# Kernel optimization log

Measured on AMD Instinct MI355X. Metric: run time of the kernel, lower is better.

Reference implementation:

```python
import jax, jax.numpy as jnp
import numpy as np

DIM = 96
HEADS = 6
WS = 8                      # window_size
OWS = int(WS * 0.5) + WS    # overlap_win_size = 12
PAD = (OWS - WS) // 2       # 2
Dd = Hh = Ww = 24
B = 1
L = Dd * Hh * Ww
MLP_H = DIM * 2
TBL = (WS + OWS - 1) ** 3   # 6859 relative-position-bias entries


def setup_inputs() -> dict:
    key = jax.random.key(0)
    ks = jax.random.split(key, 8)
    def n(k, shape, s=0.02):
        return jax.random.normal(k, shape, jnp.float32) * s
    return {
        "x": jax.random.normal(ks[0], (B, L, DIM), jnp.float32),
        "ln1_w": jnp.ones((DIM,), jnp.float32),
        "ln1_b": jnp.zeros((DIM,), jnp.float32),
        "qkv_w": n(ks[1], (3 * DIM, DIM)),
        "qkv_b": jnp.zeros((3 * DIM,), jnp.float32),
        "rpb": n(ks[2], (TBL, HEADS)),
        "proj_w": n(ks[3], (DIM, DIM)),
        "proj_b": jnp.zeros((DIM,), jnp.float32),
        "ln2_w": jnp.ones((DIM,), jnp.float32),
        "ln2_b": jnp.zeros((DIM,), jnp.float32),
        "fc1_w": n(ks[4], (MLP_H, DIM)),
        "fc1_b": jnp.zeros((MLP_H,), jnp.float32),
        "fc2_w": n(ks[5], (DIM, MLP_H)),
        "fc2_b": jnp.zeros((DIM,), jnp.float32),
        "rpi": jax.random.randint(ks[6], (WS ** 3, OWS ** 3), 0, TBL),
        "D": Dd, "H": Hh, "W": Ww,
    }


def _ln(x, w, b):
    m = jnp.mean(x, -1, keepdims=True)
    v = jnp.var(x, -1, keepdims=True)
    return (x - m) / jnp.sqrt(v + 1e-5) * w + b


def _ocab3d(x, ln1_w, ln1_b, qkv_w, qkv_b, rpb, proj_w, proj_b,
            ln2_w, ln2_b, fc1_w, fc1_b, fc2_w, fc2_b, rpi, D, H, W):
    Bz, Lz, C = x.shape
    hd = C // HEADS
    scale = hd ** -0.5
    shortcut = x

    xn = _ln(x, ln1_w, ln1_b).reshape(Bz, D, H, W, C)
    qkv = xn @ qkv_w.T + qkv_b                   # [B,D,H,W,3C]
    q = qkv[..., :C]
    kv = qkv[..., C:]                            # cat(k, v) on channels, [B,D,H,W,2C]

    nD, nH, nW = D // WS, H // WS, W // WS
    nw = nD * nH * nW

    # non-overlapping query windows -> [B*nw, WS^3, C]
    qw = q.reshape(Bz, nD, WS, nH, WS, nW, WS, C)
    qw = qw.transpose(0, 1, 3, 5, 2, 4, 6, 7).reshape(Bz * nw, WS ** 3, C)

    # overlapping kv windows via pad + strided gather (mirrors F.pad + unfold)
    kvp = jnp.pad(kv, ((0, 0), (PAD, PAD), (PAD, PAD), (PAD, PAD), (0, 0)))
    idx_d = (jnp.arange(nD) * WS)[:, None] + jnp.arange(OWS)[None, :]
    idx_h = (jnp.arange(nH) * WS)[:, None] + jnp.arange(OWS)[None, :]
    idx_w = (jnp.arange(nW) * WS)[:, None] + jnp.arange(OWS)[None, :]
    kw = kvp[:, idx_d]                 # [B,nD,OWS,Hp,Wp,2C]
    kw = kw[:, :, :, idx_h]            # [B,nD,OWS,nH,OWS,Wp,2C]
    kw = kw[:, :, :, :, :, idx_w]      # [B,nD,OWS,nH,OWS,nW,OWS,2C]
    kw = kw.transpose(0, 1, 3, 5, 2, 4, 6, 7).reshape(Bz * nw, OWS ** 3, 2 * C)
    kk, vv = kw[..., :C], kw[..., C:]

    qh = qw.reshape(-1, WS ** 3, HEADS, hd).transpose(0, 2, 1, 3) * scale
    kh = kk.reshape(-1, OWS ** 3, HEADS, hd).transpose(0, 2, 1, 3)
    vh = vv.reshape(-1, OWS ** 3, HEADS, hd).transpose(0, 2, 1, 3)

    attn = jnp.einsum('bhqd,bhkd->bhqk', qh, kh)               # [B*nw,H,512,1728]
    bias = rpb[rpi.reshape(-1)].reshape(WS ** 3, OWS ** 3, HEADS).transpose(2, 0, 1)
    attn = jax.nn.softmax(attn + bias[None], axis=-1)
    out = jnp.einsum('bhqk,bhkd->bhqd', attn, vh)
    out = out.transpose(0, 2, 1, 3).reshape(Bz * nw, WS ** 3, C)

    # window reverse -> [B, L, C]
    out = out.reshape(Bz, nD, nH, nW, WS, WS, WS, C)
    out = out.transpose(0, 1, 4, 2, 5, 3, 6, 7).reshape(Bz, D * H * W, C)

    x2 = out @ proj_w.T + proj_b + shortcut
    h1 = jax.nn.gelu(_ln(x2, ln2_w, ln2_b) @ fc1_w.T + fc1_b, approximate=False)
    return x2 + (h1 @ fc2_w.T + fc2_b)


def reference(x, ln1_w, ln1_b, qkv_w, qkv_b, rpb, proj_w, proj_b,
              ln2_w, ln2_b, fc1_w, fc1_b, fc2_w, fc2_b, rpi, D, H, W):
    return _ocab3d(x, ln1_w, ln1_b, qkv_w, qkv_b, rpb, proj_w, proj_b,
                   ln2_w, ln2_b, fc1_w, fc1_b, fc2_w, fc2_b, rpi, D, H, W)
```

## Files before the change

kernel.cpp:

```cpp
#include <hip/hip_runtime.h>
#include <math.h>

#define DIMC   96
#define NHEADS 6
#define HD     16
#define WSZ    8
#define OWSZ   12
#define PADW   2
#define DD     24
#define LTOK   13824
#define NWIN   27
#define NKEY   1728
#define NROW   512
#define MLPH   192
#define PDIM   28
#define PD3    21952
#define TBL    6859
#define LSTR   82944
#define AOSTR  1327104
#define LOG2E  1.4426950408889634f

typedef __attribute__((ext_vector_type(4))) short bf16x4;
typedef __attribute__((ext_vector_type(8))) short bf16x8;
typedef __attribute__((ext_vector_type(4))) float f32x4;

__device__ __forceinline__ unsigned short bfround(float f) {
    unsigned u = __float_as_uint(f);
    return (unsigned short)((u + 0x7FFFu + ((u >> 16) & 1u)) >> 16);
}
__device__ __forceinline__ unsigned bfpack(float a, float b) {
    unsigned ua = __float_as_uint(a), ub = __float_as_uint(b);
    ua = (ua + 0x7FFFu + ((ua >> 16) & 1u)) >> 16;
    ub = (ub + 0x7FFFu + ((ub >> 16) & 1u)) >> 16;
    return ua | (ub << 16);
}
__device__ __forceinline__ uint4 pack8(const float* v) {
    uint4 u;
    u.x = bfpack(v[0], v[1]); u.y = bfpack(v[2], v[3]);
    u.z = bfpack(v[4], v[5]); u.w = bfpack(v[6], v[7]);
    return u;
}
__device__ __forceinline__ bf16x4 pack4(f32x4 p) {
    union { uint2 u; bf16x4 v; } r;
    r.u.x = __builtin_amdgcn_perm(__float_as_uint(p[1]), __float_as_uint(p[0]), 0x07060302u);
    r.u.y = __builtin_amdgcn_perm(__float_as_uint(p[3]), __float_as_uint(p[2]), 0x07060302u);
    return r.v;
}
__device__ __forceinline__ f32x4 cvt4(uint2 b) {
    f32x4 c;
    c[0] = __uint_as_float(b.x << 16);
    c[1] = __uint_as_float(b.x & 0xffff0000u);
    c[2] = __uint_as_float(b.y << 16);
    c[3] = __uint_as_float(b.y & 0xffff0000u);
    return c;
}
__device__ __forceinline__ f32x4 mfma16(bf16x4 a, bf16x4 b, f32x4 c) {
#if __has_builtin(__builtin_amdgcn_mfma_f32_16x16x16bf16_1k)
    return __builtin_amdgcn_mfma_f32_16x16x16bf16_1k(a, b, c, 0, 0, 0);
#else
    bf16x8 a8 = {a[0], a[1], a[2], a[3], 0, 0, 0, 0};
    bf16x8 b8 = {b[0], b[1], b[2], b[3], 0, 0, 0, 0};
    return __builtin_amdgcn_mfma_f32_16x16x32_bf16(a8, b8, c, 0, 0, 0);
#endif
}
__device__ __forceinline__ f32x4 mfma32k(bf16x8 a, bf16x8 b, f32x4 c) {
    return __builtin_amdgcn_mfma_f32_16x16x32_bf16(a, b, c, 0, 0, 0);
}
__device__ __forceinline__ float fexp2(float x) {
#if __has_builtin(__builtin_amdgcn_exp2f)
    return __builtin_amdgcn_exp2f(x);
#else
    return exp2f(x);
#endif
}

#define QKVB 1296
#define ZB   515
#define WPB  45
#define BIASB 216
__global__ __launch_bounds__(256) void qkvz_kernel(
        const float* __restrict__ X, const float* __restrict__ W,
        const float* __restrict__ bias, const float* __restrict__ lnw,
        const float* __restrict__ lnb,
        const float* __restrict__ projw, const float* __restrict__ fc1w,
        const float* __restrict__ fc2w,
        const int* __restrict__ rpi, const float* __restrict__ rpb,
        unsigned short* __restrict__ q16, unsigned short* __restrict__ kvp2,
        uint4* __restrict__ wpack, unsigned short* __restrict__ biasP) {
    __shared__ uint4 Af4[2 * 3 * 4 * 16];
    __shared__ uint4 Bf4[6 * 3 * 4 * 16];
    int bx = blockIdx.x, tid = threadIdx.x;

    if (bx >= QKVB + ZB + WPB) {
        int b2 = bx - (QKVB + ZB + WPB);
        int c  = b2 % 27;
        int qp = b2 / 27;
        int quart = qp >> 1, qt = qp & 1;
        int wavep = tid >> 6, quadp = (tid >> 4) & 3, m16p = tid & 15;
        int q = quart * 128 + wavep * 32 + qt * 16 + m16p;
        const int* rp = rpi + (long)q * NKEY + c * 64 + quadp * 8;
        #pragma unroll
        for (int kt = 0; kt < 4; ++kt) {
            int4 t = *(const int4*)(rp + (kt >> 1) * 32 + (kt & 1) * 4);
            const float2* p0 = (const float2*)(rpb + (long)t.x * 6);
            const float2* p1 = (const float2*)(rpb + (long)t.y * 6);
            const float2* p2 = (const float2*)(rpb + (long)t.z * 6);
            const float2* p3 = (const float2*)(rpb + (long)t.w * 6);
            #pragma unroll
            for (int hp = 0; hp < 3; ++hp) {
                float2 a0 = p0[hp], a1 = p1[hp], a2 = p2[hp], a3 = p3[hp];
                uint2 ua, ub;
                ua.x = bfpack(a0.x * LOG2E, a1.x * LOG2E);
                ua.y = bfpack(a2.x * LOG2E, a3.x * LOG2E);
                ub.x = bfpack(a0.y * LOG2E, a1.y * LOG2E);
                ub.y = bfpack(a2.y * LOG2E, a3.y * LOG2E);
                *(uint2*)(biasP + ((long)((2*hp)   * 4 + quart) * 27 + c) * 8192
                          + qt * 4096 + tid * 16 + kt * 4) = ua;
                *(uint2*)(biasP + ((long)((2*hp+1) * 4 + quart) * 27 + c) * 8192
                          + qt * 4096 + tid * 16 + kt * 4) = ub;
            }
        }
        return;
    }
    if (bx >= QKVB + ZB) {
        int u = (bx - QKVB - ZB) * 256 + tid;
        if (u < 5760) {
            int p = (u < 1152) ? u : (u < 3456 ? (u - 1152) % 1152 : (u - 3456) % 1152);
            int nn = p & 15, r = p >> 4, qg = r & 3, r2 = r >> 2;
            int kt = r2 % 3, ct = r2 / 3;
            int n = ct * 16 + nn, g = kt * 4 + qg;
            const float* src;
            if (u < 1152)      src = projw + n * 96 + g * 8;
            else if (u < 3456) { int nc = (u - 1152) / 1152; src = fc1w + (long)(nc * 96 + n) * 96 + g * 8; }
            else               { int kh = (u - 3456) / 1152; src = fc2w + (long)n * 192 + kh * 96 + g * 8; }
            const float4* s4 = (const float4*)src;
            float v[8];
            float4 t0 = s4[0], t1 = s4[1];
            v[0]=t0.x; v[1]=t0.y; v[2]=t0.z; v[3]=t0.w;
            v[4]=t1.x; v[5]=t1.y; v[6]=t1.z; v[7]=t1.w;
            wpack[u] = pack8(v);
        }
        return;
    }
    if (bx >= QKVB) {
        int t = (bx - QKVB) * 256 + tid;
        if (t < 21952 * 6) {
            int head = t / PD3, pos = t % PD3;
            int d = pos / 784, h = (pos / 28) % 28, w = pos % 28;
            if (d < 2 || d >= 26 || h < 2 || h >= 26 || w < 2 || w >= 26) {
                uint4* p = (uint4*)(kvp2 + ((long)head * PD3 + pos) * 32);
                uint4 z = make_uint4(0, 0, 0, 0);
                p[0] = z; p[1] = z; p[2] = z; p[3] = z;
            }
        }
        return;
    }

    int nc   = bx % 3;
    int row0 = (bx / 3) * 32;

    if (tid < 128) {
        int row = tid >> 2, part = tid & 3;
        int rt = row >> 4, mm = row & 15;
        float v[24];
        const float4* xp = (const float4*)(X + (long)(row0 + row) * 96 + part * 24);
        float s = 0.f, sq = 0.f;
        #pragma unroll
        for (int i = 0; i < 6; ++i) {
            float4 t = xp[i];
            v[i*4+0] = t.x; v[i*4+1] = t.y; v[i*4+2] = t.z; v[i*4+3] = t.w;
            s  += t.x + t.y + t.z + t.w;
            sq += t.x*t.x + t.y*t.y + t.z*t.z + t.w*t.w;
        }
        s  += __shfl_xor(s, 1);  s  += __shfl_xor(s, 2);
        sq += __shfl_xor(sq, 1); sq += __shfl_xor(sq, 2);
        float mean = s * (1.f / 96.f);
        float inv  = rsqrtf(sq * (1.f / 96.f) - mean * mean + 1e-5f);
        const float4* wp = (const float4*)(lnw + part * 24);
        const float4* bp = (const float4*)(lnb + part * 24);
        #pragma unroll
        for (int i = 0; i < 6; ++i) {
            float4 wv = wp[i], bv = bp[i];
            v[i*4+0] = (v[i*4+0] - mean) * inv * wv.x + bv.x;
            v[i*4+1] = (v[i*4+1] - mean) * inv * wv.y + bv.y;
            v[i*4+2] = (v[i*4+2] - mean) * inv * wv.z + bv.z;
            v[i*4+3] = (v[i*4+3] - mean) * inv * wv.w + bv.w;
        }
        #pragma unroll
        for (int gg = 0; gg < 3; ++gg) {
            int g = part * 3 + gg;
            int kt = g >> 2, qq = g & 3;
            Af4[((rt * 3 + kt) * 4 + qq) * 16 + mm] = pack8(v + gg * 8);
        }
    }
    for (int idx = tid; idx < 96 * 12; idx += 256) {
        int n = idx / 12;
        int g = idx % 12;
        const float4* wp = (const float4*)(W + (long)(nc * 96 + n) * 96 + g * 8);
        float v[8];
        float4 t0 = wp[0], t1 = wp[1];
        v[0]=t0.x; v[1]=t0.y; v[2]=t0.z; v[3]=t0.w;
        v[4]=t1.x; v[5]=t1.y; v[6]=t1.z; v[7]=t1.w;
        int ct = n >> 4, nn = n & 15, kt = g >> 2, qg = g & 3;
        Bf4[((ct * 3 + kt) * 4 + qg) * 16 + nn] = pack8(v);
    }
    __syncthreads();

    int wave = tid >> 6, lane = tid & 63;
    int qq = lane >> 4, mI = lane & 15;
    int rt = wave & 1, cg = wave >> 1;

    f32x4 acc[3];
    #pragma unroll
    for (int j = 0; j < 3; ++j) acc[j] = (f32x4){0.f, 0.f, 0.f, 0.f};
    #pragma unroll
    for (int kt = 0; kt < 3; ++kt) {
        bf16x8 a = *(const bf16x8*)&Af4[((rt * 3 + kt) * 4 + qq) * 16 + mI];
        #pragma unroll
        for (int j = 0; j < 3; ++j) {
            bf16x8 b = *(const bf16x8*)&Bf4[(((cg * 3 + j) * 3 + kt) * 4 + qq) * 16 + mI];
            acc[j] = __builtin_amdgcn_mfma_f32_16x16x32_bf16(a, b, acc[j], 0, 0, 0);
        }
    }

    float bv[3];
    #pragma unroll
    for (int j = 0; j < 3; ++j) bv[j] = bias[nc * 96 + (cg * 3 + j) * 16 + mI];
    #pragma unroll
    for (int r = 0; r < 4; ++r) {
        int row = row0 + rt * 16 + qq * 4 + r;
        if (nc == 0) {
            unsigned short* op = q16 + (long)row * 96;
            #pragma unroll
            for (int j = 0; j < 3; ++j)
                op[(cg * 3 + j) * 16 + mI] = bfround(0.25f * LOG2E * (acc[j][r] + bv[j]));
        } else {
            int d = row / 576, hh = (row / 24) % 24, w2 = row % 24;
            long pos = ((long)(d + 2) * 28 + (hh + 2)) * 28 + (w2 + 2);
            #pragma unroll
            for (int j = 0; j < 3; ++j) {
                int head = cg * 3 + j;
                kvp2[((long)head * PD3 + pos) * 32 +
                     (nc == 2 ? 16 : 0) + mI] = bfround(acc[j][r] + bv[j]);
            }
        }
    }
}

#define KSTR 20
#define VKP  66

#define ATTN_STEP(P, BCUR, BNXT)                                              \
    {                                                                         \
        bool more = (cc + (P) + 1 < cn);                                      \
        if (more) stgn = *kvaddr(c0 + cc + (P) + 1);                          \
        __syncthreads();                                                      \
        bf16x4 kf[4];                                                         \
        _Pragma("unroll")                                                     \
        for (int kt = 0; kt < 4; ++kt)                                        \
            kf[kt] = *(const bf16x4*)&Ks[(P)][(kt * 16 + m16) * KSTR + quad * 4]; \
        bf16x8 vb0 = *(const bf16x8*)&Vt[(P)][m16 * VKP + quad * 8];          \
        bf16x8 vb1 = *(const bf16x8*)&Vt[(P)][m16 * VKP + 32 + quad * 8];     \
        f32x4 S[2][4];                                                        \
        _Pragma("unroll")                                                     \
        for (int qt = 0; qt < 2; ++qt) {                                      \
            _Pragma("unroll")                                                 \
            for (int kt = 0; kt < 4; ++kt) {                                  \
                uint4 bj = BCUR[qt][kt >> 1];                                 \
                uint2 bb = (kt & 1) ? make_uint2(bj.z, bj.w)                  \
                                    : make_uint2(bj.x, bj.y);                 \
                S[qt][kt] = mfma16(kf[kt], qf[qt], cvt4(bb));                 \
            }                                                                 \
        }                                                                     \
        if (more) {                                                           \
            const unsigned short* bp = bbase + (long)(c0 + cc + (P) + 1) * 8192 \
                                       + tid * 16;                            \
            _Pragma("unroll")                                                 \
            for (int qt = 0; qt < 2; ++qt) {                                  \
                BNXT[qt][0] = *(const uint4*)(bp + qt * 4096);                \
                BNXT[qt][1] = *(const uint4*)(bp + qt * 4096 + 8);            \
            }                                                                 \
        }                                                                     \
        bf16x8 P8[2][2];                                                      \
        _Pragma("unroll")                                                     \
        for (int qt = 0; qt < 2; ++qt) {                                      \
            _Pragma("unroll")                                                 \
            for (int u = 0; u < 2; ++u) {                                     \
                f32x4 p0, p1;                                                 \
                _Pragma("unroll")                                             \
                for (int r = 0; r < 4; ++r) {                                 \
                    p0[r] = fexp2(S[qt][2 * u][r]);                           \
                    p1[r] = fexp2(S[qt][2 * u + 1][r]);                       \
                }                                                             \
                union { struct { bf16x4 lo, hi; } h; bf16x8 v; } uu;          \
                uu.h.lo = pack4(p0); uu.h.hi = pack4(p1);                     \
                P8[qt][u] = uu.v;                                             \
                lacc[qt] = mfma32k(P8[qt][u], ones8, lacc[qt]);               \
            }                                                                 \
        }                                                                     \
        o[0] = mfma32k(P8[0][0], vb0, o[0]);                                  \
        o[1] = mfma32k(P8[1][0], vb0, o[1]);                                  \
        o[0] = mfma32k(P8[0][1], vb1, o[0]);                                  \
        o[1] = mfma32k(P8[1][1], vb1, o[1]);                                  \
        if (more) writeLDS((P) ^ 1, stgn);                                    \
    }

__global__ __launch_bounds__(256, 3) void attn_kernel(
        const unsigned short* __restrict__ q, const unsigned short* __restrict__ kvp2,
        const unsigned short* __restrict__ biasP, float* __restrict__ ao,
        float* __restrict__ lbuf) {
    __shared__ unsigned short Ks[2][64 * KSTR];
    __shared__ unsigned short Vt[2][16 * VKP];
    int bid = blockIdx.x;
    int w = bid / 48, rem = bid % 48;
    int head = rem >> 3;
    int quart = (rem >> 1) & 3, half = rem & 1;
    int wd8 = (w / 9) * 8, wh8 = ((w / 3) % 3) * 8, ww8 = (w % 3) * 8;
    int tid = threadIdx.x, wave = tid >> 6, lane = tid & 63;
    int quad = lane >> 4, m16 = lane & 15;
    int key = tid >> 2, part = tid & 3;
    int c0 = half ? 13 : 0;
    int cn = half ? 14 : 13;

    int skey = (key & 35) | ((key & 4) << 2) | ((key >> 1) & 12);

    auto kvaddr = [&](int c) -> const uint4* {
        int jg = c * 64 + key;
        int i = jg / 144, jh = (jg / 12) % 12, jw = jg % 12;
        long sp = ((long)(wd8 + i) * PDIM + (wh8 + jh)) * PDIM + (ww8 + jw);
        return (const uint4*)(kvp2 + ((long)head * PD3 + sp) * 32 + part * 8);
    };
    auto writeLDS = [&](int b, uint4 v) {
        if (part < 2) {
            *(uint2*)(&Ks[b][skey * KSTR + part * 8])     = make_uint2(v.x, v.y);
            *(uint2*)(&Ks[b][skey * KSTR + part * 8 + 4]) = make_uint2(v.z, v.w);
        } else {
            int d0 = (part - 2) * 8;
            unsigned short* vp = &Vt[b][d0 * VKP + key];
            vp[0 * VKP] = (unsigned short)(v.x);
            vp[1 * VKP] = (unsigned short)(v.x >> 16);
            vp[2 * VKP] = (unsigned short)(v.y);
            vp[3 * VKP] = (unsigned short)(v.y >> 16);
            vp[4 * VKP] = (unsigned short)(v.z);
            vp[5 * VKP] = (unsigned short)(v.z >> 16);
            vp[6 * VKP] = (unsigned short)(v.w);
            vp[7 * VKP] = (unsigned short)(v.w >> 16);
        }
    };

    bf16x4 qf[2];
    #pragma unroll
    for (int qt = 0; qt < 2; ++qt) {
        int ql = quart * 128 + wave * 32 + qt * 16 + m16;
        int ld = ql >> 6, lh = (ql >> 3) & 7, lw = ql & 7;
        int g = ((wd8 + ld) * 24 + (wh8 + lh)) * 24 + (ww8 + lw);
        qf[qt] = *(const bf16x4*)(q + (long)g * 96 + head * 16 + quad * 4);
    }

    const unsigned short* bbase = biasP + ((long)(head * 4 + quart) * 27) * 8192;
    uint4 bb0[2][2], bb1[2][2];
    {
        const unsigned short* bp = bbase + (long)c0 * 8192 + tid * 16;
        #pragma unroll
        for (int qt = 0; qt < 2; ++qt) {
            bb0[qt][0] = *(const uint4*)(bp + qt * 4096);
            bb0[qt][1] = *(const uint4*)(bp + qt * 4096 + 8);
        }
    }

    writeLDS(0, *kvaddr(c0));

    const bf16x8 ones8 = {(short)0x3F80, (short)0x3F80, (short)0x3F80, (short)0x3F80,
                          (short)0x3F80, (short)0x3F80, (short)0x3F80, (short)0x3F80};
    f32x4 o[2], lacc[2];
    o[0] = (f32x4){0.f,0.f,0.f,0.f}; o[1] = (f32x4){0.f,0.f,0.f,0.f};
    lacc[0] = o[0]; lacc[1] = o[1];
    uint4 stgn;

    for (int cc = 0; cc < cn; cc += 2) {
        ATTN_STEP(0, bb0, bb1)
        if (cc + 1 < cn) ATTN_STEP(1, bb1, bb0)
    }

    float* aout = ao + (long)half * AOSTR;
    float* lout = lbuf + (long)half * LSTR;
    #pragma unroll
    for (int qt = 0; qt < 2; ++qt) {
        #pragma unroll
        for (int r = 0; r < 4; ++r) {
            int ql = quart * 128 + wave * 32 + qt * 16 + quad * 4 + r;
            int ld = ql >> 6, lh = (ql >> 3) & 7, lw = ql & 7;
            int g = ((wd8 + ld) * 24 + (wh8 + lh)) * 24 + (ww8 + lw);
            aout[(long)g * 96 + head * 16 + m16] = o[qt][r];
            if (m16 == 0) lout[g * 6 + head] = lacc[qt][r];
        }
    }
}

#define X2S 100
__global__ __launch_bounds__(512) void mlp_kernel(
        const float* __restrict__ ao0, const float* __restrict__ ao1,
        const float* __restrict__ lbuf, const uint4* __restrict__ wpack,
        const float* __restrict__ projb, const float* __restrict__ x,
        const float* __restrict__ ln2w, const float* __restrict__ ln2b,
        const float* __restrict__ fc1b, const float* __restrict__ fc2b,
        float* __restrict__ out) {
    __shared__ uint4 Ws[5760];
    __shared__ uint4 Af4[4 * 3 * 4 * 16];
    __shared__ float x2s[64 * X2S];
    __shared__ unsigned short h16[64 * 192];
    int tid = threadIdx.x;
    int row0 = blockIdx.x * 64;
    int wave = tid >> 6, lane = tid & 63;
    int qq = lane >> 4, mI = lane & 15;
    int rt = wave & 3, cg = wave >> 2;

    for (int idx = tid; idx < 5760; idx += 512) Ws[idx] = wpack[idx];

    if (tid < 256) {
        int row = tid >> 2, part = tid & 3;
        int rtA = row >> 4, mm = row & 15;
        int grow = row0 + row;
        const float4* a0 = (const float4*)(ao0 + (long)grow * 96 + part * 24);
        const float4* a1 = (const float4*)(ao1 + (long)grow * 96 + part * 24);
        int ha = (part * 3) >> 1, hb = ha + 1;
        float inva = 1.f / (lbuf[grow*6 + ha] + lbuf[LSTR + grow*6 + ha]);
        float invb = 1.f / (lbuf[grow*6 + hb] + lbuf[LSTR + grow*6 + hb]);
        float v[24];
        #pragma unroll
        for (int i = 0; i < 6; ++i) {
            float4 u0 = a0[i], u1 = a1[i];
            #pragma unroll
            for (int j = 0; j < 4; ++j) {
                int gc = part * 24 + i * 4 + j;
                float lv = ((gc >> 4) == ha) ? inva : invb;
                float s = (j==0?u0.x+u1.x : j==1?u0.y+u1.y : j==2?u0.z+u1.z : u0.w+u1.w);
                v[i*4+j] = s * lv;
            }
        }
        #pragma unroll
        for (int gg = 0; gg < 3; ++gg) {
            int g = part * 3 + gg;
            int kt = g >> 2, q4 = g & 3;
            Af4[((rtA * 3 + kt) * 4 + q4) * 16 + mm] = pack8(v + gg * 8);
        }
    }
    __syncthreads();

    {
        f32x4 acc[3];
        #pragma unroll
        for (int j = 0; j < 3; ++j) acc[j] = (f32x4){0.f,0.f,0.f,0.f};
        #pragma unroll
        for (int kt = 0; kt < 3; ++kt) {
            bf16x8 a = *(const bf16x8*)&Af4[((rt * 3 + kt) * 4 + qq) * 16 + mI];
            #pragma unroll
            for (int j = 0; j < 3; ++j) {
                bf16x8 b = *(const bf16x8*)&Ws[(((cg * 3 + j) * 3 + kt) * 4 + qq) * 16 + mI];
                acc[j] = __builtin_amdgcn_mfma_f32_16x16x32_bf16(a, b, acc[j], 0, 0, 0);
            }
        }
        float bv[3];
        #pragma unroll
        for (int j = 0; j < 3; ++j) bv[j] = projb[(cg * 3 + j) * 16 + mI];
        #pragma unroll
        for (int r = 0; r < 4; ++r) {
            int row = rt * 16 + qq * 4 + r;
            int grow = row0 + row;
            #pragma unroll
            for (int j = 0; j < 3; ++j) {
                int col = (cg * 3 + j) * 16 + mI;
                x2s[row * X2S + col] = acc[j][r] + bv[j] + x[(long)grow * 96 + col];
            }
        }
    }
    __syncthreads();

    if (tid < 256) {
        int row = tid >> 2, part = tid & 3;
        int rtA = row >> 4, mm = row & 15;
        float v[24];
        const float4* xp = (const float4*)(x2s + row * X2S + part * 24);
        float s = 0.f, sq = 0.f;
        #pragma unroll
        for (int i = 0; i < 6; ++i) {
            float4 t = xp[i];
            v[i*4+0] = t.x; v[i*4+1] = t.y; v[i*4+2] = t.z; v[i*4+3] = t.w;
            s  += t.x + t.y + t.z + t.w;
            sq += t.x*t.x + t.y*t.y + t.z*t.z + t.w*t.w;
        }
        s  += __shfl_xor(s, 1);  s  += __shfl_xor(s, 2);
        sq += __shfl_xor(sq, 1); sq += __shfl_xor(sq, 2);
        float mean = s * (1.f / 96.f);
        float inv  = rsqrtf(sq * (1.f / 96.f) - mean * mean + 1e-5f);
        const float4* wp = (const float4*)(ln2w + part * 24);
        const float4* bp = (const float4*)(ln2b + part * 24);
        #pragma unroll
        for (int i = 0; i < 6; ++i) {
            float4 wv = wp[i], bv = bp[i];
            v[i*4+0] = (v[i*4+0] - mean) * inv * wv.x + bv.x;
            v[i*4+1] = (v[i*4+1] - mean) * inv * wv.y + bv.y;
            v[i*4+2] = (v[i*4+2] - mean) * inv * wv.z + bv.z;
            v[i*4+3] = (v[i*4+3] - mean) * inv * wv.w + bv.w;
        }
        #pragma unroll
        for (int gg = 0; gg < 3; ++gg) {
            int g = part * 3 + gg;
            int kt = g >> 2, q4 = g & 3;
            Af4[((rtA * 3 + kt) * 4 + q4) * 16 + mm] = pack8(v + gg * 8);
        }
    }
    __syncthreads();

    #pragma unroll
    for (int nc = 0; nc < 2; ++nc) {
        f32x4 acc[3];
        #pragma unroll
        for (int j = 0; j < 3; ++j) acc[j] = (f32x4){0.f,0.f,0.f,0.f};
        #pragma unroll
        for (int kt = 0; kt < 3; ++kt) {
            bf16x8 a = *(const bf16x8*)&Af4[((rt * 3 + kt) * 4 + qq) * 16 + mI];
            #pragma unroll
            for (int j = 0; j < 3; ++j) {
                bf16x8 b = *(const bf16x8*)&Ws[1152 + nc * 1152 +
                               (((cg * 3 + j) * 3 + kt) * 4 + qq) * 16 + mI];
                acc[j] = __builtin_amdgcn_mfma_f32_16x16x32_bf16(a, b, acc[j], 0, 0, 0);
            }
        }
        float bv[3];
        #pragma unroll
        for (int j = 0; j < 3; ++j) bv[j] = fc1b[nc * 96 + (cg * 3 + j) * 16 + mI];
        #pragma unroll
        for (int r = 0; r < 4; ++r) {
            int row = rt * 16 + qq * 4 + r;
            #pragma unroll
            for (int j = 0; j < 3; ++j) {
                int col = nc * 96 + (cg * 3 + j) * 16 + mI;
                float v = acc[j][r] + bv[j];
                float g = 0.5f * v * (1.f + erff(v * 0.70710678f));
                int fi = (((row >> 4) * 6 + (col >> 5)) * 4 + ((col >> 3) & 3)) * 16 + (row & 15);
                h16[fi * 8 + (col & 7)] = bfround(g);
            }
        }
    }
    __syncthreads();

    f32x4 acc2[3];
    #pragma unroll
    for (int j = 0; j < 3; ++j) acc2[j] = (f32x4){0.f,0.f,0.f,0.f};
    #pragma unroll
    for (int kh = 0; kh < 2; ++kh) {
        #pragma unroll
        for (int kt = 0; kt < 3; ++kt) {
            int ktA = kh * 3 + kt;
            bf16x8 a = *(const bf16x8*)&h16[(((rt * 6 + ktA) * 4 + qq) * 16 + mI) * 8];
            #pragma unroll
            for (int j = 0; j < 3; ++j) {
                bf16x8 b = *(const bf16x8*)&Ws[3456 + kh * 1152 +
                               (((cg * 3 + j) * 3 + kt) * 4 + qq) * 16 + mI];
                acc2[j] = __builtin_amdgcn_mfma_f32_16x16x32_bf16(a, b, acc2[j], 0, 0, 0);
            }
        }
    }
    float bv[3];
    #pragma unroll
    for (int j = 0; j < 3; ++j) bv[j] = fc2b[(cg * 3 + j) * 16 + mI];
    #pragma unroll
    for (int r = 0; r < 4; ++r) {
        int row = rt * 16 + qq * 4 + r;
        int grow = row0 + row;
        #pragma unroll
        for (int j = 0; j < 3; ++j) {
            int col = (cg * 3 + j) * 16 + mI;
            out[(long)grow * 96 + col] = acc2[j][r] + bv[j] + x2s[row * X2S + col];
        }
    }
}

extern "C" void kernel_launch(void* const* d_in, const int* in_sizes, int n_in,
                              void* d_out, int out_size, void* d_ws, size_t ws_size,
                              hipStream_t stream) {
    const float* x     = (const float*)d_in[0];
    const float* ln1w  = (const float*)d_in[1];
    const float* ln1b  = (const float*)d_in[2];
    const float* qkvw  = (const float*)d_in[3];
    const float* qkvb  = (const float*)d_in[4];
    const float* rpb   = (const float*)d_in[5];
    const float* projw = (const float*)d_in[6];
    const float* projb = (const float*)d_in[7];
    const float* ln2w  = (const float*)d_in[8];
    const float* ln2b  = (const float*)d_in[9];
    const float* fc1w  = (const float*)d_in[10];
    const float* fc1b  = (const float*)d_in[11];
    const float* fc2w  = (const float*)d_in[12];
    const float* fc2b  = (const float*)d_in[13];
    const int*   rpi   = (const int*)d_in[14];
    float* outp = (float*)d_out;

    float* ws = (float*)d_ws;
    float*          aop    = ws;
    unsigned short* q16    = (unsigned short*)(ws + 2654208);
    unsigned short* kvp16  = (unsigned short*)(ws + 3317760);
    unsigned short* biasPh = (unsigned short*)(ws + 5425152);
    float*          lbuf   = ws + 10733568;
    uint4*          wpack  = (uint4*)(ws + 10899456);

    qkvz_kernel<<<QKVB + ZB + WPB + BIASB, 256, 0, stream>>>(
        x, qkvw, qkvb, ln1w, ln1b, projw, fc1w, fc2w, rpi, rpb,
        q16, kvp16, wpack, biasPh);
    attn_kernel<<<NWIN * NHEADS * 4 * 2, 256, 0, stream>>>(q16, kvp16, biasPh, aop, lbuf);
    mlp_kernel<<<LTOK / 64, 512, 0, stream>>>(aop, aop + AOSTR, lbuf, wpack, projb, x,
                                              ln2w, ln2b, fc1b, fc2b, outp);
}
```

Baseline: 158.8 us.

## Split attention blocks per query tile, read MLP weights from global, vectorize bias gather

```diff
diff --git a/kernel.cpp b/kernel.cpp
--- a/kernel.cpp
+++ b/kernel.cpp
@@ -102,23 +102,34 @@
         #pragma unroll
         for (int kt = 0; kt < 4; ++kt) {
             int4 t = *(const int4*)(rp + (kt >> 1) * 32 + (kt & 1) * 4);
-            const float2* p0 = (const float2*)(rpb + (long)t.x * 6);
-            const float2* p1 = (const float2*)(rpb + (long)t.y * 6);
-            const float2* p2 = (const float2*)(rpb + (long)t.z * 6);
-            const float2* p3 = (const float2*)(rpb + (long)t.w * 6);
-            #pragma unroll
-            for (int hp = 0; hp < 3; ++hp) {
-                float2 a0 = p0[hp], a1 = p1[hp], a2 = p2[hp], a3 = p3[hp];
-                uint2 ua, ub;
-                ua.x = bfpack(a0.x * LOG2E, a1.x * LOG2E);
-                ua.y = bfpack(a2.x * LOG2E, a3.x * LOG2E);
-                ub.x = bfpack(a0.y * LOG2E, a1.y * LOG2E);
-                ub.y = bfpack(a2.y * LOG2E, a3.y * LOG2E);
-                *(uint2*)(biasP + ((long)((2*hp)   * 4 + quart) * 27 + c) * 8192
-                          + qt * 4096 + tid * 16 + kt * 4) = ua;
-                *(uint2*)(biasP + ((long)((2*hp+1) * 4 + quart) * 27 + c) * 8192
-                          + qt * 4096 + tid * 16 + kt * 4) = ub;
-            }
+            const float* b0 = rpb + (long)t.x * 6;
+            const float* b1 = rpb + (long)t.y * 6;
+            const float* b2p = rpb + (long)t.z * 6;
+            const float* b3 = rpb + (long)t.w * 6;
+            float4 q0 = *(const float4*)b0; float2 r0 = *(const float2*)(b0 + 4);
+            float4 q1 = *(const float4*)b1; float2 r1 = *(const float2*)(b1 + 4);
+            float4 q2 = *(const float4*)b2p; float2 r2 = *(const float2*)(b2p + 4);
+            float4 q3 = *(const float4*)b3; float2 r3 = *(const float2*)(b3 + 4);
+            long ob = qt * 4096 + tid * 16 + kt * 4;
+            uint2 ua, ub;
+            ua.x = bfpack(q0.x * LOG2E, q1.x * LOG2E);
+            ua.y = bfpack(q2.x * LOG2E, q3.x * LOG2E);
+            ub.x = bfpack(q0.y * LOG2E, q1.y * LOG2E);
+            ub.y = bfpack(q2.y * LOG2E, q3.y * LOG2E);
+            *(uint2*)(biasP + ((long)(0 * 4 + quart) * 27 + c) * 8192 + ob) = ua;
+            *(uint2*)(biasP + ((long)(1 * 4 + quart) * 27 + c) * 8192 + ob) = ub;
+            ua.x = bfpack(q0.z * LOG2E, q1.z * LOG2E);
+            ua.y = bfpack(q2.z * LOG2E, q3.z * LOG2E);
+            ub.x = bfpack(q0.w * LOG2E, q1.w * LOG2E);
+            ub.y = bfpack(q2.w * LOG2E, q3.w * LOG2E);
+            *(uint2*)(biasP + ((long)(2 * 4 + quart) * 27 + c) * 8192 + ob) = ua;
+            *(uint2*)(biasP + ((long)(3 * 4 + quart) * 27 + c) * 8192 + ob) = ub;
+            ua.x = bfpack(r0.x * LOG2E, r1.x * LOG2E);
+            ua.y = bfpack(r2.x * LOG2E, r3.x * LOG2E);
+            ub.x = bfpack(r0.y * LOG2E, r1.y * LOG2E);
+            ub.y = bfpack(r2.y * LOG2E, r3.y * LOG2E);
+            *(uint2*)(biasP + ((long)(4 * 4 + quart) * 27 + c) * 8192 + ob) = ua;
+            *(uint2*)(biasP + ((long)(5 * 4 + quart) * 27 + c) * 8192 + ob) = ub;
         }
         return;
     }
@@ -261,60 +272,49 @@
             kf[kt] = *(const bf16x4*)&Ks[(P)][(kt * 16 + m16) * KSTR + quad * 4]; \
         bf16x8 vb0 = *(const bf16x8*)&Vt[(P)][m16 * VKP + quad * 8];          \
         bf16x8 vb1 = *(const bf16x8*)&Vt[(P)][m16 * VKP + 32 + quad * 8];     \
-        f32x4 S[2][4];                                                        \
+        f32x4 S[4];                                                           \
         _Pragma("unroll")                                                     \
-        for (int qt = 0; qt < 2; ++qt) {                                      \
-            _Pragma("unroll")                                                 \
-            for (int kt = 0; kt < 4; ++kt) {                                  \
-                uint4 bj = BCUR[qt][kt >> 1];                                 \
-                uint2 bb = (kt & 1) ? make_uint2(bj.z, bj.w)                  \
-                                    : make_uint2(bj.x, bj.y);                 \
-                S[qt][kt] = mfma16(kf[kt], qf[qt], cvt4(bb));                 \
-            }                                                                 \
+        for (int kt = 0; kt < 4; ++kt) {                                      \
+            uint4 bj = BCUR[kt >> 1];                                         \
+            uint2 bb = (kt & 1) ? make_uint2(bj.z, bj.w)                      \
+                                : make_uint2(bj.x, bj.y);                     \
+            S[kt] = mfma16(kf[kt], qf, cvt4(bb));                             \
         }                                                                     \
         if (more) {                                                           \
             const unsigned short* bp = bbase + (long)(c0 + cc + (P) + 1) * 8192 \
                                        + tid * 16;                            \
+            BNXT[0] = *(const uint4*)(bp);                                    \
+            BNXT[1] = *(const uint4*)(bp + 8);                                \
+        }                                                                     \
+        bf16x8 P8[2];                                                         \
+        _Pragma("unroll")                                                     \
+        for (int u = 0; u < 2; ++u) {                                         \
+            f32x4 p0, p1;                                                     \
             _Pragma("unroll")                                                 \
-            for (int qt = 0; qt < 2; ++qt) {                                  \
-                BNXT[qt][0] = *(const uint4*)(bp + qt * 4096);                \
-                BNXT[qt][1] = *(const uint4*)(bp + qt * 4096 + 8);            \
+            for (int r = 0; r < 4; ++r) {                                     \
+                p0[r] = fexp2(S[2 * u][r]);                                   \
+                p1[r] = fexp2(S[2 * u + 1][r]);                               \
             }                                                                 \
+            union { struct { bf16x4 lo, hi; } h; bf16x8 v; } uu;              \
+            uu.h.lo = pack4(p0); uu.h.hi = pack4(p1);                         \
+            P8[u] = uu.v;                                                     \
+            lacc = mfma32k(P8[u], ones8, lacc);                               \
         }                                                                     \
-        bf16x8 P8[2][2];                                                      \
-        _Pragma("unroll")                                                     \
-        for (int qt = 0; qt < 2; ++qt) {                                      \
-            _Pragma("unroll")                                                 \
-            for (int u = 0; u < 2; ++u) {                                     \
-                f32x4 p0, p1;                                                 \
-                _Pragma("unroll")                                             \
-                for (int r = 0; r < 4; ++r) {                                 \
-                    p0[r] = fexp2(S[qt][2 * u][r]);                           \
-                    p1[r] = fexp2(S[qt][2 * u + 1][r]);                       \
-                }                                                             \
-                union { struct { bf16x4 lo, hi; } h; bf16x8 v; } uu;          \
-                uu.h.lo = pack4(p0); uu.h.hi = pack4(p1);                     \
-                P8[qt][u] = uu.v;                                             \
-                lacc[qt] = mfma32k(P8[qt][u], ones8, lacc[qt]);               \
-            }                                                                 \
-        }                                                                     \
-        o[0] = mfma32k(P8[0][0], vb0, o[0]);                                  \
-        o[1] = mfma32k(P8[1][0], vb0, o[1]);                                  \
-        o[0] = mfma32k(P8[0][1], vb1, o[0]);                                  \
-        o[1] = mfma32k(P8[1][1], vb1, o[1]);                                  \
+        o = mfma32k(P8[0], vb0, o);                                           \
+        o = mfma32k(P8[1], vb1, o);                                           \
         if (more) writeLDS((P) ^ 1, stgn);                                    \
     }
 
-__global__ __launch_bounds__(256, 3) void attn_kernel(
+__global__ __launch_bounds__(256, 4) void attn_kernel(
         const unsigned short* __restrict__ q, const unsigned short* __restrict__ kvp2,
         const unsigned short* __restrict__ biasP, float* __restrict__ ao,
         float* __restrict__ lbuf) {
     __shared__ unsigned short Ks[2][64 * KSTR];
     __shared__ unsigned short Vt[2][16 * VKP];
     int bid = blockIdx.x;
-    int w = bid / 48, rem = bid % 48;
-    int head = rem >> 3;
-    int quart = (rem >> 1) & 3, half = rem & 1;
+    int w = bid / 96, rem = bid % 96;
+    int head = rem >> 4;
+    int quart = (rem >> 2) & 3, qt = (rem >> 1) & 1, half = rem & 1;
     int wd8 = (w / 9) * 8, wh8 = ((w / 3) % 3) * 8, ww8 = (w % 3) * 8;
     int tid = threadIdx.x, wave = tid >> 6, lane = tid & 63;
     int quad = lane >> 4, m16 = lane & 15;
@@ -348,33 +348,29 @@
         }
     };
 
-    bf16x4 qf[2];
-    #pragma unroll
-    for (int qt = 0; qt < 2; ++qt) {
+    bf16x4 qf;
+    {
         int ql = quart * 128 + wave * 32 + qt * 16 + m16;
         int ld = ql >> 6, lh = (ql >> 3) & 7, lw = ql & 7;
         int g = ((wd8 + ld) * 24 + (wh8 + lh)) * 24 + (ww8 + lw);
-        qf[qt] = *(const bf16x4*)(q + (long)g * 96 + head * 16 + quad * 4);
-    }
-
-    const unsigned short* bbase = biasP + ((long)(head * 4 + quart) * 27) * 8192;
-    uint4 bb0[2][2], bb1[2][2];
+        qf = *(const bf16x4*)(q + (long)g * 96 + head * 16 + quad * 4);
+    }
+
+    const unsigned short* bbase = biasP + ((long)(head * 4 + quart) * 27) * 8192
+                                  + qt * 4096;
+    uint4 bb0[2], bb1[2];
     {
         const unsigned short* bp = bbase + (long)c0 * 8192 + tid * 16;
-        #pragma unroll
-        for (int qt = 0; qt < 2; ++qt) {
-            bb0[qt][0] = *(const uint4*)(bp + qt * 4096);
-            bb0[qt][1] = *(const uint4*)(bp + qt * 4096 + 8);
-        }
+        bb0[0] = *(const uint4*)(bp);
+        bb0[1] = *(const uint4*)(bp + 8);
     }
 
     writeLDS(0, *kvaddr(c0));
 
     const bf16x8 ones8 = {(short)0x3F80, (short)0x3F80, (short)0x3F80, (short)0x3F80,
                           (short)0x3F80, (short)0x3F80, (short)0x3F80, (short)0x3F80};
-    f32x4 o[2], lacc[2];
-    o[0] = (f32x4){0.f,0.f,0.f,0.f}; o[1] = (f32x4){0.f,0.f,0.f,0.f};
-    lacc[0] = o[0]; lacc[1] = o[1];
+    f32x4 o = (f32x4){0.f,0.f,0.f,0.f};
+    f32x4 lacc = (f32x4){0.f,0.f,0.f,0.f};
     uint4 stgn;
 
     for (int cc = 0; cc < cn; cc += 2) {
@@ -385,15 +381,12 @@
     float* aout = ao + (long)half * AOSTR;
     float* lout = lbuf + (long)half * LSTR;
     #pragma unroll
-    for (int qt = 0; qt < 2; ++qt) {
-        #pragma unroll
-        for (int r = 0; r < 4; ++r) {
-            int ql = quart * 128 + wave * 32 + qt * 16 + quad * 4 + r;
-            int ld = ql >> 6, lh = (ql >> 3) & 7, lw = ql & 7;
-            int g = ((wd8 + ld) * 24 + (wh8 + lh)) * 24 + (ww8 + lw);
-            aout[(long)g * 96 + head * 16 + m16] = o[qt][r];
-            if (m16 == 0) lout[g * 6 + head] = lacc[qt][r];
-        }
+    for (int r = 0; r < 4; ++r) {
+        int ql = quart * 128 + wave * 32 + qt * 16 + quad * 4 + r;
+        int ld = ql >> 6, lh = (ql >> 3) & 7, lw = ql & 7;
+        int g = ((wd8 + ld) * 24 + (wh8 + lh)) * 24 + (ww8 + lw);
+        aout[(long)g * 96 + head * 16 + m16] = o[r];
+        if (m16 == 0) lout[g * 6 + head] = lacc[r];
     }
 }
 
@@ -405,7 +398,6 @@
         const float* __restrict__ ln2w, const float* __restrict__ ln2b,
         const float* __restrict__ fc1b, const float* __restrict__ fc2b,
         float* __restrict__ out) {
-    __shared__ uint4 Ws[5760];
     __shared__ uint4 Af4[4 * 3 * 4 * 16];
     __shared__ float x2s[64 * X2S];
     __shared__ unsigned short h16[64 * 192];
@@ -414,8 +406,6 @@
     int wave = tid >> 6, lane = tid & 63;
     int qq = lane >> 4, mI = lane & 15;
     int rt = wave & 3, cg = wave >> 2;
-
-    for (int idx = tid; idx < 5760; idx += 512) Ws[idx] = wpack[idx];
 
     if (tid < 256) {
         int row = tid >> 2, part = tid & 3;
@@ -456,7 +446,7 @@
             bf16x8 a = *(const bf16x8*)&Af4[((rt * 3 + kt) * 4 + qq) * 16 + mI];
             #pragma unroll
             for (int j = 0; j < 3; ++j) {
-                bf16x8 b = *(const bf16x8*)&Ws[(((cg * 3 + j) * 3 + kt) * 4 + qq) * 16 + mI];
+                bf16x8 b = *(const bf16x8*)&wpack[(((cg * 3 + j) * 3 + kt) * 4 + qq) * 16 + mI];
                 acc[j] = __builtin_amdgcn_mfma_f32_16x16x32_bf16(a, b, acc[j], 0, 0, 0);
             }
         }
@@ -522,7 +512,7 @@
             bf16x8 a = *(const bf16x8*)&Af4[((rt * 3 + kt) * 4 + qq) * 16 + mI];
             #pragma unroll
             for (int j = 0; j < 3; ++j) {
-                bf16x8 b = *(const bf16x8*)&Ws[1152 + nc * 1152 +
+                bf16x8 b = *(const bf16x8*)&wpack[1152 + nc * 1152 +
                                (((cg * 3 + j) * 3 + kt) * 4 + qq) * 16 + mI];
                 acc[j] = __builtin_amdgcn_mfma_f32_16x16x32_bf16(a, b, acc[j], 0, 0, 0);
             }
@@ -556,7 +546,7 @@
             bf16x8 a = *(const bf16x8*)&h16[(((rt * 6 + ktA) * 4 + qq) * 16 + mI) * 8];
             #pragma unroll
             for (int j = 0; j < 3; ++j) {
-                bf16x8 b = *(const bf16x8*)&Ws[3456 + kh * 1152 +
+                bf16x8 b = *(const bf16x8*)&wpack[3456 + kh * 1152 +
                                (((cg * 3 + j) * 3 + kt) * 4 + qq) * 16 + mI];
                 acc2[j] = __builtin_amdgcn_mfma_f32_16x16x32_bf16(a, b, acc2[j], 0, 0, 0);
             }
@@ -608,7 +598,7 @@
     qkvz_kernel<<<QKVB + ZB + WPB + BIASB, 256, 0, stream>>>(
         x, qkvw, qkvb, ln1w, ln1b, projw, fc1w, fc2w, rpi, rpb,
         q16, kvp16, wpack, biasPh);
-    attn_kernel<<<NWIN * NHEADS * 4 * 2, 256, 0, stream>>>(q16, kvp16, biasPh, aop, lbuf);
+    attn_kernel<<<NWIN * NHEADS * 16, 256, 0, stream>>>(q16, kvp16, biasPh, aop, lbuf);
     mlp_kernel<<<LTOK / 64, 512, 0, stream>>>(aop, aop + AOSTR, lbuf, wpack, projb, x,
                                               ln2w, ln2b, fc1b, fc2b, outp);
 }
```

Result: no change. 159.9 us (+0.7%).
